# Performance work log

Measured on AMD Instinct MI355X. Metric: run time of the kernel, lower is better.

Reference implementation:

```python
import jax, jax.numpy as jnp
import numpy as np

EPS = 1e-3          # posdef_tol
CRLB = 1.0          # contraction_rate_lb
STD = 0.5           # initialization_std
DX, L, DIN, DOUT, B = 512, 512, 256, 256, 8192


def setup_inputs() -> dict:
    key = jax.random.key(0)
    ks = jax.random.split(key, 9)
    f32 = jnp.float32
    return {
        "u_in": jax.random.normal(ks[0], (B, 1, DIN), f32),
        "x0": jnp.zeros((B, 1, DX), f32),
        "X": jax.random.normal(ks[1], (2 * DX + L, 2 * DX + L), f32) * STD,
        "Y": jax.random.normal(ks[2], (DX, DX), f32) * STD,
        "B2": jax.random.normal(ks[3], (DX, DIN), f32) * STD,
        "C2": jax.random.normal(ks[4], (DOUT, DX), f32) * STD,
        "D21": jax.random.normal(ks[5], (DOUT, L), f32) * STD,
        "D22": jax.random.normal(ks[6], (DOUT, DIN), f32) * STD,
        "D12": jax.random.normal(ks[7], (L, DIN), f32) * STD,
    }


def _derive(X, Y, dx, l):
    # update_model_param: H = X^T X + eps*I, then block-split
    H = X.T @ X + EPS * jnp.eye(2 * dx + l, dtype=X.dtype)
    H11 = H[:dx, :dx]
    H21 = H[dx:dx + l, :dx]
    H22 = H[dx:dx + l, dx:dx + l]
    H31 = H[dx + l:, :dx]
    H32 = H[dx + l:, dx:dx + l]
    H33 = H[dx + l:, dx + l:]
    Fm = H31
    B1 = H32
    E = 0.5 * (H11 + CRLB * H33 + Y - Y.T)
    Lam = 0.5 * jnp.diag(H22)
    D11 = -jnp.tril(H22, -1)   # strictly lower triangular
    C1 = -H21
    return Fm, B1, E, Lam, D11, C1


def reference(u_in, x0, X, Y, B2, C2, D21, D22, D12):
    b = u_in.shape[0]
    dx = x0.shape[-1]
    l = D12.shape[0]
    u = u_in[:, 0, :]          # (B, din)
    x = x0[:, 0, :]            # (B, dx)
    Fm, B1, E, Lam, D11, C1 = _derive(X, Y, dx, l)

    # v_i = C1[i]@x + D11[i]@w + D12[i]@u ; the x/u parts are loop-invariant
    a = x @ C1.T + u @ D12.T   # (B, l)

    def step(w, inputs):
        a_i, d_row, lam_i, e_row = inputs
        v = a_i + w @ d_row                       # (B,) forward substitution
        w = w + jnp.tanh(v / lam_i)[:, None] * e_row[None, :]
        return w, None

    eye = jnp.eye(l, dtype=u.dtype)
    w0 = jnp.zeros((b, l), u.dtype)
    w, _ = jax.lax.scan(step, w0, (a.T, D11, Lam, eye))  # (B, l)

    pre = x @ Fm.T + w @ B1.T + u @ B2.T          # (B, dx)
    # F.linear(pre, E^{-1}) = pre @ E^{-T} = solve(E, pre^T)^T
    x_new = jnp.linalg.solve(E, pre.T).T          # (B, dx)
    y = x_new @ C2.T + w @ D21.T + u @ D22.T      # (B, dout)
    return y[:, None, :]                          # (B, 1, dout)
```

## Files before the change

kernel.cpp:

```cpp
#include <hip/hip_runtime.h>
#include <cstdint>
#include <cstddef>

#define EPSC 0.001f

typedef __attribute__((ext_vector_type(8))) short short8;
typedef __attribute__((ext_vector_type(4))) float f32x4;

__device__ inline void bsplit(float f, ushort& h, ushort& l) {
  uint b = __float_as_uint(f);
  h = (ushort)(b >> 16);
  float r = f - __uint_as_float(b & 0xFFFF0000u);
  l = (ushort)(__float_as_uint(r) >> 16);
}

__global__ void k_anynz(const float* __restrict__ x, int n4, int* __restrict__ flag) {
  int i = blockIdx.x * blockDim.x + threadIdx.x;
  int stride = gridDim.x * blockDim.x;
  int found = 0;
  for (; i < n4; i += stride) {
    float4 v = ((const float4*)x)[i];
    if (v.x != 0.f || v.y != 0.f || v.z != 0.f || v.w != 0.f) { found = 1; break; }
  }
  if (found) atomicOr(flag, 1);
}

__global__ __launch_bounds__(256) void k_tsplit(const float* __restrict__ src,
    ushort* __restrict__ dh, ushort* __restrict__ dl, int R, int C)
{
  __shared__ float t[32][33];
  const int c0 = blockIdx.x * 32, r0 = blockIdx.y * 32;
  const int tid = threadIdx.x;
  const int lr = tid >> 3, lc4 = (tid & 7) * 4;
  float4 v = *(const float4*)(src + (size_t)(r0 + lr) * C + c0 + lc4);
  t[lr][lc4 + 0] = v.x; t[lr][lc4 + 1] = v.y;
  t[lr][lc4 + 2] = v.z; t[lr][lc4 + 3] = v.w;
  __syncthreads();
  ushort4 hv, lv;
  float f;
  f = t[lc4 + 0][lr]; bsplit(f, hv.x, lv.x);
  f = t[lc4 + 1][lr]; bsplit(f, hv.y, lv.y);
  f = t[lc4 + 2][lr]; bsplit(f, hv.z, lv.z);
  f = t[lc4 + 3][lr]; bsplit(f, hv.w, lv.w);
  size_t off = (size_t)(c0 + lr) * R + r0 + lc4;
  *(ushort4*)(dh + off) = hv;
  *(ushort4*)(dl + off) = lv;
}

__global__ void k_split2(const float* __restrict__ s0, ushort* __restrict__ h0,
                         ushort* __restrict__ l0, int c0,
                         const float* __restrict__ s1, ushort* __restrict__ h1,
                         ushort* __restrict__ l1, int c1)
{
  int i = blockIdx.x * 256 + threadIdx.x;
  int tot = c0 + c1;
  int stride = gridDim.x * 256;
  for (; i < tot; i += stride) {
    const float* s; ushort* h; ushort* l; int k;
    if (i < c0) { s = s0; h = h0; l = l0; k = i; }
    else        { s = s1; h = h1; l = l1; k = i - c0; }
    float4 v = ((const float4*)s)[k];
    ushort4 hv, lv;
    bsplit(v.x, hv.x, lv.x);
    bsplit(v.y, hv.y, lv.y);
    bsplit(v.z, hv.z, lv.z);
    bsplit(v.w, hv.w, lv.w);
    ((ushort4*)h)[k] = hv;
    ((ushort4*)l)[k] = lv;
  }
}

__global__ __launch_bounds__(256) void k_xtxm(
    const ushort* __restrict__ Xth, const ushort* __restrict__ Xtl,
    const float* __restrict__ Y,
    float* __restrict__ E, float* __restrict__ C1,
    float* __restrict__ D11, float* __restrict__ D11T, float* __restrict__ Lam,
    ushort* __restrict__ FmTh, ushort* __restrict__ FmTl,
    ushort* __restrict__ B1Th, ushort* __restrict__ B1Tl)
{
  __shared__ ushort sAh[64][40], sAl[64][40], sBh[64][40], sBl[64][40];
  const int z = blockIdx.z;
  int aOff[2], bOff[2], nops;
  switch (z) {
    case 0:  aOff[0] = 0;    bOff[0] = 0;    aOff[1] = 1024; bOff[1] = 1024; nops = 2; break;
    case 1:  aOff[0] = 512;  bOff[0] = 0;    nops = 1; break;
    case 2:  aOff[0] = 512;  bOff[0] = 512;  nops = 1; break;
    case 3:  aOff[0] = 0;    bOff[0] = 1024; nops = 1; break;
    default: aOff[0] = 512;  bOff[0] = 1024; nops = 1; break;
  }
  const int tid = threadIdx.x;
  const int m0 = blockIdx.x * 64, n0 = blockIdx.y * 64;
  const int wid = tid >> 6, lane = tid & 63;
  const int wr = wid >> 1, wc = wid & 1;
  const int fr = lane & 15, fg = lane >> 4;
  const int srow = tid >> 2;
  const int sko = (tid & 3) * 8;
  f32x4 acc[2][2] = {};
  const int K = 1536;

  for (int op = 0; op < nops; ++op) {
    const ushort* Ah = Xth + (size_t)(aOff[op]) * K;
    const ushort* Al = Xtl + (size_t)(aOff[op]) * K;
    const ushort* Bh = Xth + (size_t)(bOff[op]) * K;
    const ushort* Bl = Xtl + (size_t)(bOff[op]) * K;
    uint4 pah = *(const uint4*)(Ah + (size_t)(m0 + srow) * K + sko);
    uint4 pal = *(const uint4*)(Al + (size_t)(m0 + srow) * K + sko);
    uint4 pbh = *(const uint4*)(Bh + (size_t)(n0 + srow) * K + sko);
    uint4 pbl = *(const uint4*)(Bl + (size_t)(n0 + srow) * K + sko);
    for (int k0 = 0; k0 < K; k0 += 32) {
      __syncthreads();
      *(uint4*)&sAh[srow][sko] = pah;
      *(uint4*)&sAl[srow][sko] = pal;
      *(uint4*)&sBh[srow][sko] = pbh;
      *(uint4*)&sBl[srow][sko] = pbl;
      __syncthreads();
      if (k0 + 32 < K) {
        pah = *(const uint4*)(Ah + (size_t)(m0 + srow) * K + k0 + 32 + sko);
        pal = *(const uint4*)(Al + (size_t)(m0 + srow) * K + k0 + 32 + sko);
        pbh = *(const uint4*)(Bh + (size_t)(n0 + srow) * K + k0 + 32 + sko);
        pbl = *(const uint4*)(Bl + (size_t)(n0 + srow) * K + k0 + 32 + sko);
      }
      short8 fah[2], fal[2], fbh[2], fbl[2];
#pragma unroll
      for (int s = 0; s < 2; ++s) {
        fah[s] = *(const short8*)&sAh[wr * 32 + s * 16 + fr][fg * 8];
        fal[s] = *(const short8*)&sAl[wr * 32 + s * 16 + fr][fg * 8];
        fbh[s] = *(const short8*)&sBh[wc * 32 + s * 16 + fr][fg * 8];
        fbl[s] = *(const short8*)&sBl[wc * 32 + s * 16 + fr][fg * 8];
      }
#pragma unroll
      for (int i = 0; i < 2; ++i)
#pragma unroll
        for (int j = 0; j < 2; ++j) {
          acc[i][j] = __builtin_amdgcn_mfma_f32_16x16x32_bf16(fah[i], fbh[j], acc[i][j], 0, 0, 0);
          acc[i][j] = __builtin_amdgcn_mfma_f32_16x16x32_bf16(fah[i], fbl[j], acc[i][j], 0, 0, 0);
          acc[i][j] = __builtin_amdgcn_mfma_f32_16x16x32_bf16(fal[i], fbh[j], acc[i][j], 0, 0, 0);
        }
    }
  }

#pragma unroll
  for (int i = 0; i < 2; ++i)
#pragma unroll
    for (int j = 0; j < 2; ++j) {
      int rbase = m0 + wr * 32 + i * 16 + fg * 4;
      int cc = n0 + wc * 32 + j * 16 + fr;
#pragma unroll
      for (int q = 0; q < 4; ++q) {
        int rr = rbase + q;
        float d = acc[i][j][q];
        size_t idx = (size_t)rr * 512 + cc;
        if (z == 0) {
          float o = 0.5f * (d + Y[idx] - Y[(size_t)cc * 512 + rr]);
          if (rr == cc) o += EPSC;
          E[idx] = o;
        } else if (z == 1) {
          C1[idx] = -d;
        } else if (z == 2) {
          float o = (cc < rr) ? -d : 0.f;
          D11[idx] = o;
          D11T[(size_t)cc * 512 + rr] = o;
          if (rr == cc) Lam[rr] = 0.5f * (d + EPSC);
        } else if (z == 3) {
          ushort h, l; bsplit(d, h, l);
          FmTh[idx] = h; FmTl[idx] = l;
        } else {
          ushort h, l; bsplit(d, h, l);
          B1Th[idx] = h; B1Tl[idx] = l;
        }
      }
    }
}

__global__ void k_nsinit(const float* __restrict__ E, const float* __restrict__ C2,
    float* __restrict__ Tf, ushort* __restrict__ Th, ushort* __restrict__ Tl,
    ushort* __restrict__ Tth, ushort* __restrict__ Ttl,
    float* __restrict__ Qf, ushort* __restrict__ Qh, ushort* __restrict__ Ql)
{
  int g = blockIdx.x * 256 + threadIdx.x;
  int row = g >> 7;
  int c4 = (g & 127) << 2;
  float s0 = 0.85f / E[(size_t)(c4 + 0) * 513];
  float s1 = 0.85f / E[(size_t)(c4 + 1) * 513];
  float s2 = 0.85f / E[(size_t)(c4 + 2) * 513];
  float s3 = 0.85f / E[(size_t)(c4 + 3) * 513];
  if (row < 512) {
    float4 v = *(const float4*)(E + (size_t)row * 512 + c4);
    v.x *= s0; v.y *= s1; v.z *= s2; v.w *= s3;
    *(float4*)(Tf + (size_t)row * 512 + c4) = v;
    ushort4 hv, lv;
    bsplit(v.x, hv.x, lv.x); bsplit(v.y, hv.y, lv.y);
    bsplit(v.z, hv.z, lv.z); bsplit(v.w, hv.w, lv.w);
    *(ushort4*)(Th + (size_t)row * 512 + c4) = hv;
    *(ushort4*)(Tl + (size_t)row * 512 + c4) = lv;
    Tth[(size_t)(c4 + 0) * 512 + row] = hv.x; Ttl[(size_t)(c4 + 0) * 512 + row] = lv.x;
    Tth[(size_t)(c4 + 1) * 512 + row] = hv.y; Ttl[(size_t)(c4 + 1) * 512 + row] = lv.y;
    Tth[(size_t)(c4 + 2) * 512 + row] = hv.z; Ttl[(size_t)(c4 + 2) * 512 + row] = lv.z;
    Tth[(size_t)(c4 + 3) * 512 + row] = hv.w; Ttl[(size_t)(c4 + 3) * 512 + row] = lv.w;
  } else {
    int qr = row - 512;
    float4 v = *(const float4*)(C2 + (size_t)qr * 512 + c4);
    v.x *= s0; v.y *= s1; v.z *= s2; v.w *= s3;
    *(float4*)(Qf + (size_t)qr * 512 + c4) = v;
    ushort4 hv, lv;
    bsplit(v.x, hv.x, lv.x); bsplit(v.y, hv.y, lv.y);
    bsplit(v.z, hv.z, lv.z); bsplit(v.w, hv.w, lv.w);
    *(ushort4*)(Qh + (size_t)qr * 512 + c4) = hv;
    *(ushort4*)(Ql + (size_t)qr * 512 + c4) = lv;
  }
}

template <bool WITH_T>
__global__ __launch_bounds__(256) void k_nsm(
    const ushort* __restrict__ Th, const ushort* __restrict__ Tl,
    const ushort* __restrict__ Tth, const ushort* __restrict__ Ttl,
    const ushort* __restrict__ Qh, const ushort* __restrict__ Ql,
    const float* __restrict__ Tprev, const float* __restrict__ Qprev,
    float* __restrict__ Tnext, ushort* __restrict__ Thn, ushort* __restrict__ Tln,
    ushort* __restrict__ Tthn, ushort* __restrict__ Ttln,
    float* __restrict__ Qnext, ushort* __restrict__ Qhn, ushort* __restrict__ Qln)
{
  __shared__ ushort sAh[64][40], sAl[64][40], sBh[64][40], sBl[64][40];
  const int tid = threadIdx.x;
  const int yy = blockIdx.y;
  const bool isT = WITH_T && (yy < 8);
  const int m0 = (isT ? yy : (yy - (WITH_T ? 8 : 0))) * 64;
  const int n0 = blockIdx.x * 64;
  const ushort* Ah = isT ? Th : Qh;
  const ushort* Al = isT ? Tl : Ql;
  const int wid = tid >> 6, lane = tid & 63;
  const int wr = wid >> 1, wc = wid & 1;
  const int fr = lane & 15, fg = lane >> 4;
  const int srow = tid >> 2;
  const int sko = (tid & 3) * 8;
  const int K = 512;
  f32x4 acc[2][2] = {};

  uint4 pah = *(const uint4*)(Ah + (size_t)(m0 + srow) * K + sko);
  uint4 pal = *(const uint4*)(Al + (size_t)(m0 + srow) * K + sko);
  uint4 pbh = *(const uint4*)(Tth + (size_t)(n0 + srow) * K + sko);
  uint4 pbl = *(const uint4*)(Ttl + (size_t)(n0 + srow) * K + sko);
  for (int k0 = 0; k0 < K; k0 += 32) {
    __syncthreads();
    *(uint4*)&sAh[srow][sko] = pah;
    *(uint4*)&sAl[srow][sko] = pal;
    *(uint4*)&sBh[srow][sko] = pbh;
    *(uint4*)&sBl[srow][sko] = pbl;
    __syncthreads();
    if (k0 + 32 < K) {
      pah = *(const uint4*)(Ah + (size_t)(m0 + srow) * K + k0 + 32 + sko);
      pal = *(const uint4*)(Al + (size_t)(m0 + srow) * K + k0 + 32 + sko);
      pbh = *(const uint4*)(Tth + (size_t)(n0 + srow) * K + k0 + 32 + sko);
      pbl = *(const uint4*)(Ttl + (size_t)(n0 + srow) * K + k0 + 32 + sko);
    }
    short8 fah[2], fal[2], fbh[2], fbl[2];
#pragma unroll
    for (int s = 0; s < 2; ++s) {
      fah[s] = *(const short8*)&sAh[wr * 32 + s * 16 + fr][fg * 8];
      fal[s] = *(const short8*)&sAl[wr * 32 + s * 16 + fr][fg * 8];
      fbh[s] = *(const short8*)&sBh[wc * 32 + s * 16 + fr][fg * 8];
      fbl[s] = *(const short8*)&sBl[wc * 32 + s * 16 + fr][fg * 8];
    }
#pragma unroll
    for (int i = 0; i < 2; ++i)
#pragma unroll
      for (int j = 0; j < 2; ++j) {
        acc[i][j] = __builtin_amdgcn_mfma_f32_16x16x32_bf16(fah[i], fbh[j], acc[i][j], 0, 0, 0);
        acc[i][j] = __builtin_amdgcn_mfma_f32_16x16x32_bf16(fah[i], fbl[j], acc[i][j], 0, 0, 0);
        acc[i][j] = __builtin_amdgcn_mfma_f32_16x16x32_bf16(fal[i], fbh[j], acc[i][j], 0, 0, 0);
      }
  }

#pragma unroll
  for (int i = 0; i < 2; ++i)
#pragma unroll
    for (int j = 0; j < 2; ++j) {
      int rbase = m0 + wr * 32 + i * 16 + fg * 4;
      int cc = n0 + wc * 32 + j * 16 + fr;
#pragma unroll
      for (int q = 0; q < 4; ++q) {
        int rr = rbase + q;
        size_t idx = (size_t)rr * 512 + cc;
        ushort h, l;
        if (isT) {
          float tn = 2.f * Tprev[idx] - acc[i][j][q];
          Tnext[idx] = tn;
          bsplit(tn, h, l);
          Thn[idx] = h; Tln[idx] = l;
          Tthn[(size_t)cc * 512 + rr] = h; Ttln[(size_t)cc * 512 + rr] = l;
        } else {
          float qn = 2.f * Qprev[idx] - acc[i][j][q];
          Qnext[idx] = qn;
          bsplit(qn, h, l);
          Qhn[idx] = h; Qln[idx] = l;
        }
      }
    }
}

__global__ __launch_bounds__(256) void k_foldm(
    const ushort* __restrict__ Qh, const ushort* __restrict__ Ql,
    const ushort* __restrict__ FmTh, const ushort* __restrict__ FmTl,
    const ushort* __restrict__ B1Th, const ushort* __restrict__ B1Tl,
    const ushort* __restrict__ B2Th, const ushort* __restrict__ B2Tl,
    const float* __restrict__ D21, const float* __restrict__ D22,
    float* __restrict__ P1, ushort* __restrict__ P2h, ushort* __restrict__ P2l,
    ushort* __restrict__ P3h, ushort* __restrict__ P3l)
{
  __shared__ ushort sAh[64][40], sAl[64][40], sBh[64][40], sBl[64][40];
  const int z = blockIdx.z;
  const int N = (z == 2) ? 256 : 512;
  const int n0 = blockIdx.x * 64;
  if (n0 >= N) return;
  const ushort* Bh = (z == 0) ? FmTh : (z == 1) ? B1Th : B2Th;
  const ushort* Bl = (z == 0) ? FmTl : (z == 1) ? B1Tl : B2Tl;
  const int tid = threadIdx.x;
  const int m0 = blockIdx.y * 64;
  const int wid = tid >> 6, lane = tid & 63;
  const int wr = wid >> 1, wc = wid & 1;
  const int fr = lane & 15, fg = lane >> 4;
  const int srow = tid >> 2;
  const int sko = (tid & 3) * 8;
  const int K = 512;
  f32x4 acc[2][2] = {};

  uint4 pah = *(const uint4*)(Qh + (size_t)(m0 + srow) * K + sko);
  uint4 pal = *(const uint4*)(Ql + (size_t)(m0 + srow) * K + sko);
  uint4 pbh = *(const uint4*)(Bh + (size_t)(n0 + srow) * K + sko);
  uint4 pbl = *(const uint4*)(Bl + (size_t)(n0 + srow) * K + sko);
  for (int k0 = 0; k0 < K; k0 += 32) {
    __syncthreads();
    *(uint4*)&sAh[srow][sko] = pah;
    *(uint4*)&sAl[srow][sko] = pal;
    *(uint4*)&sBh[srow][sko] = pbh;
    *(uint4*)&sBl[srow][sko] = pbl;
    __syncthreads();
    if (k0 + 32 < K) {
      pah = *(const uint4*)(Qh + (size_t)(m0 + srow) * K + k0 + 32 + sko);
      pal = *(const uint4*)(Ql + (size_t)(m0 + srow) * K + k0 + 32 + sko);
      pbh = *(const uint4*)(Bh + (size_t)(n0 + srow) * K + k0 + 32 + sko);
      pbl = *(const uint4*)(Bl + (size_t)(n0 + srow) * K + k0 + 32 + sko);
    }
    short8 fah[2], fal[2], fbh[2], fbl[2];
#pragma unroll
    for (int s = 0; s < 2; ++s) {
      fah[s] = *(const short8*)&sAh[wr * 32 + s * 16 + fr][fg * 8];
      fal[s] = *(const short8*)&sAl[wr * 32 + s * 16 + fr][fg * 8];
      fbh[s] = *(const short8*)&sBh[wc * 32 + s * 16 + fr][fg * 8];
      fbl[s] = *(const short8*)&sBl[wc * 32 + s * 16 + fr][fg * 8];
    }
#pragma unroll
    for (int i = 0; i < 2; ++i)
#pragma unroll
      for (int j = 0; j < 2; ++j) {
        acc[i][j] = __builtin_amdgcn_mfma_f32_16x16x32_bf16(fah[i], fbh[j], acc[i][j], 0, 0, 0);
        acc[i][j] = __builtin_amdgcn_mfma_f32_16x16x32_bf16(fah[i], fbl[j], acc[i][j], 0, 0, 0);
        acc[i][j] = __builtin_amdgcn_mfma_f32_16x16x32_bf16(fal[i], fbh[j], acc[i][j], 0, 0, 0);
      }
  }

#pragma unroll
  for (int i = 0; i < 2; ++i)
#pragma unroll
    for (int j = 0; j < 2; ++j) {
      int rbase = m0 + wr * 32 + i * 16 + fg * 4;
      int cc = n0 + wc * 32 + j * 16 + fr;
#pragma unroll
      for (int q = 0; q < 4; ++q) {
        int rr = rbase + q;
        float d = acc[i][j][q];
        if (z == 0) {
          P1[(size_t)rr * 512 + cc] = d;
        } else if (z == 1) {
          size_t idx = (size_t)rr * 512 + cc;
          float p = d + D21[idx];
          ushort h, l; bsplit(p, h, l);
          P2h[idx] = h; P2l[idx] = l;
        } else {
          size_t idx = (size_t)rr * 256 + cc;
          float p = d + D22[idx];
          ushort h, l; bsplit(p, h, l);
          P3h[idx] = h; P3l[idx] = l;
        }
      }
    }
}

template <int NOPS>
__global__ __launch_bounds__(256) void k_ntm(
    const ushort* __restrict__ Ah0, const ushort* __restrict__ Al0,
    const ushort* __restrict__ Bh0, const ushort* __restrict__ Bl0, int K0,
    const ushort* __restrict__ Ah1, const ushort* __restrict__ Al1,
    const ushort* __restrict__ Bh1, const ushort* __restrict__ Bl1, int K1,
    float* __restrict__ C, int ldc)
{
  __shared__ ushort sAh[64][40], sAl[64][40], sBh[64][40], sBl[64][40];
  const int tid = threadIdx.x;
  const int m0 = blockIdx.x * 64, n0 = blockIdx.y * 64;
  const int wid = tid >> 6, lane = tid & 63;
  const int wr = wid >> 1, wc = wid & 1;
  const int fr = lane & 15, fg = lane >> 4;
  const int srow = tid >> 2;
  const int sko = (tid & 3) * 8;
  f32x4 acc[2][2] = {};

#pragma unroll
  for (int op = 0; op < NOPS; ++op) {
    const ushort* Ah = (op == 0) ? Ah0 : Ah1;
    const ushort* Al = (op == 0) ? Al0 : Al1;
    const ushort* Bh = (op == 0) ? Bh0 : Bh1;
    const ushort* Bl = (op == 0) ? Bl0 : Bl1;
    const int K = (op == 0) ? K0 : K1;
    uint4 pah = *(const uint4*)(Ah + (size_t)(m0 + srow) * K + sko);
    uint4 pal = *(const uint4*)(Al + (size_t)(m0 + srow) * K + sko);
    uint4 pbh = *(const uint4*)(Bh + (size_t)(n0 + srow) * K + sko);
    uint4 pbl = *(const uint4*)(Bl + (size_t)(n0 + srow) * K + sko);
    for (int k0 = 0; k0 < K; k0 += 32) {
      __syncthreads();
      *(uint4*)&sAh[srow][sko] = pah;
      *(uint4*)&sAl[srow][sko] = pal;
      *(uint4*)&sBh[srow][sko] = pbh;
      *(uint4*)&sBl[srow][sko] = pbl;
      __syncthreads();
      if (k0 + 32 < K) {
        pah = *(const uint4*)(Ah + (size_t)(m0 + srow) * K + k0 + 32 + sko);
        pal = *(const uint4*)(Al + (size_t)(m0 + srow) * K + k0 + 32 + sko);
        pbh = *(const uint4*)(Bh + (size_t)(n0 + srow) * K + k0 + 32 + sko);
        pbl = *(const uint4*)(Bl + (size_t)(n0 + srow) * K + k0 + 32 + sko);
      }
      short8 fah[2], fal[2], fbh[2], fbl[2];
#pragma unroll
      for (int s = 0; s < 2; ++s) {
        fah[s] = *(const short8*)&sAh[wr * 32 + s * 16 + fr][fg * 8];
        fal[s] = *(const short8*)&sAl[wr * 32 + s * 16 + fr][fg * 8];
        fbh[s] = *(const short8*)&sBh[wc * 32 + s * 16 + fr][fg * 8];
        fbl[s] = *(const short8*)&sBl[wc * 32 + s * 16 + fr][fg * 8];
      }
#pragma unroll
      for (int i = 0; i < 2; ++i)
#pragma unroll
        for (int j = 0; j < 2; ++j) {
          acc[i][j] = __builtin_amdgcn_mfma_f32_16x16x32_bf16(fah[i], fbh[j], acc[i][j], 0, 0, 0);
          acc[i][j] = __builtin_amdgcn_mfma_f32_16x16x32_bf16(fah[i], fbl[j], acc[i][j], 0, 0, 0);
          acc[i][j] = __builtin_amdgcn_mfma_f32_16x16x32_bf16(fal[i], fbh[j], acc[i][j], 0, 0, 0);
        }
    }
  }

#pragma unroll
  for (int i = 0; i < 2; ++i)
#pragma unroll
    for (int j = 0; j < 2; ++j) {
      int rr = m0 + wr * 32 + i * 16 + fg * 4;
      int cc = n0 + wc * 32 + j * 16 + fr;
#pragma unroll
      for (int q = 0; q < 4; ++q)
        C[(size_t)(rr + q) * ldc + cc] = acc[i][j][q];
    }
}

__global__ __launch_bounds__(256) void k_ntadd(const float* __restrict__ A,
    const float* __restrict__ B, int K, const int* __restrict__ flag,
    float* __restrict__ C, int ldc)
{
  if (*flag == 0) return;
  __shared__ float As[16][68];
  __shared__ float Bs[16][68];
  const int tid = threadIdx.x;
  const int tx = tid & 15, ty = tid >> 4;
  const int m0 = blockIdx.x * 64, n0 = blockIdx.y * 64;
  const int lr = tid >> 2;
  const int lk = (tid & 3) * 4;
  float acc[4][4];
#pragma unroll
  for (int i = 0; i < 4; ++i)
#pragma unroll
    for (int j = 0; j < 4; ++j) acc[i][j] = 0.f;
  float4 av = *(const float4*)(A + (size_t)(m0 + lr) * K + lk);
  float4 bv = *(const float4*)(B + (size_t)(n0 + lr) * K + lk);
  for (int k0 = 0; k0 < K; k0 += 16) {
    __syncthreads();
    As[lk + 0][lr] = av.x; As[lk + 1][lr] = av.y;
    As[lk + 2][lr] = av.z; As[lk + 3][lr] = av.w;
    Bs[lk + 0][lr] = bv.x; Bs[lk + 1][lr] = bv.y;
    Bs[lk + 2][lr] = bv.z; Bs[lk + 3][lr] = bv.w;
    __syncthreads();
    if (k0 + 16 < K) {
      av = *(const float4*)(A + (size_t)(m0 + lr) * K + k0 + 16 + lk);
      bv = *(const float4*)(B + (size_t)(n0 + lr) * K + k0 + 16 + lk);
    }
#pragma unroll
    for (int kk = 0; kk < 16; ++kk) {
      float4 a4 = *(const float4*)&As[kk][4 * ty];
      float4 b4 = *(const float4*)&Bs[kk][4 * tx];
      float ar[4] = {a4.x, a4.y, a4.z, a4.w};
      float br[4] = {b4.x, b4.y, b4.z, b4.w};
#pragma unroll
      for (int i = 0; i < 4; ++i)
#pragma unroll
        for (int j = 0; j < 4; ++j)
          acc[i][j] = fmaf(ar[i], br[j], acc[i][j]);
    }
  }
#pragma unroll
  for (int i = 0; i < 4; ++i) {
    float* p = C + (size_t)(m0 + 4 * ty + i) * ldc + n0 + 4 * tx;
    float4 v = *(float4*)p;
    v.x += acc[i][0]; v.y += acc[i][1]; v.z += acc[i][2]; v.w += acc[i][3];
    *(float4*)p = v;
  }
}

__global__ __launch_bounds__(512, 4) void k_scan(const float* __restrict__ a,
    const float* __restrict__ D11, const float* __restrict__ D11T,
    const float* __restrict__ Lam, ushort* __restrict__ wh, ushort* __restrict__ wl)
{
  __shared__ float wt[512][17];
  __shared__ float sblk[32][17];
  __shared__ float shist[6][32][17];
  __shared__ float dblkT[2][32][33];
  __shared__ float doff[32][33];
  __shared__ float ablk[32][17];
  __shared__ float rl2[512];
  const int tid = threadIdx.x;
  const int row0 = blockIdx.x * 16;

  rl2[tid] = 2.f / Lam[tid];
  if (tid < 128) {
    int rr = tid >> 3, cq = (tid & 7) * 4;
    float4 v = *(const float4*)(a + (size_t)(row0 + rr) * 512 + cq);
    sblk[cq + 0][rr] = v.x; sblk[cq + 1][rr] = v.y;
    sblk[cq + 2][rr] = v.z; sblk[cq + 3][rr] = v.w;
  } else if (tid < 384) {
    int f = tid - 128;
    int rr = f >> 3, cq = (f & 7) * 4;
    float4 v = *(const float4*)(D11 + (size_t)rr * 512 + cq);
    dblkT[0][cq + 0][rr] = v.x; dblkT[0][cq + 1][rr] = v.y;
    dblkT[0][cq + 2][rr] = v.z; dblkT[0][cq + 3][rr] = v.w;
  }
  __syncthreads();

  for (int t = 0; t < 16; ++t) {
    const int wv = tid >> 6;
    const int lane = tid & 63;
    const int c0 = 32 * t;
    const int jend2 = 32 * (t + 1);
    if (wv == 0) {
      if (lane < 16) {
        float s[32];
#pragma unroll
        for (int il = 0; il < 32; ++il) s[il] = sblk[il][lane];
#pragma unroll
        for (int il = 0; il < 32; ++il) {
          float x2 = s[il] * rl2[c0 + il];
          float e = __expf(x2);
          float wv2 = 1.f - 2.f * __builtin_amdgcn_rcpf(e + 1.f);
          wt[c0 + il][lane] = wv2;
#pragma unroll
          for (int j2 = il + 1; j2 < 32; ++j2)
            s[j2] = fmaf(dblkT[t & 1][il][j2], wv2, s[j2]);
        }
      }
    } else if (wv <= 6) {
      if (t < 15) {
        const int r = lane & 15;
        const int il0 = (lane >> 4) * 8;
        const int n = c0;
        float acc[8] = {0.f, 0.f, 0.f, 0.f, 0.f, 0.f, 0.f, 0.f};
        for (int j0 = (wv - 1) * 4; j0 < n; j0 += 24) {
          float4 d[4][2];
          float wj4[4];
#pragma unroll
          for (int q = 0; q < 4; ++q) {
            int j = j0 + q;
            int jc = (j < n) ? j : 0;
            const float* dp = D11T + (size_t)jc * 512 + jend2 + il0;
            d[q][0] = *(const float4*)dp;
            d[q][1] = *(const float4*)(dp + 4);
            wj4[q] = (j < n) ? wt[j][r] : 0.f;
          }
#pragma unroll
          for (int q = 0; q < 4; ++q) {
            acc[0] = fmaf(d[q][0].x, wj4[q], acc[0]);
            acc[1] = fmaf(d[q][0].y, wj4[q], acc[1]);
            acc[2] = fmaf(d[q][0].z, wj4[q], acc[2]);
            acc[3] = fmaf(d[q][0].w, wj4[q], acc[3]);
            acc[4] = fmaf(d[q][1].x, wj4[q], acc[4]);
            acc[5] = fmaf(d[q][1].y, wj4[q], acc[5]);
            acc[6] = fmaf(d[q][1].z, wj4[q], acc[6]);
            acc[7] = fmaf(d[q][1].w, wj4[q], acc[7]);
          }
        }
#pragma unroll
        for (int k = 0; k < 8; ++k) shist[wv - 1][il0 + k][r] = acc[k];
      }
    } else {
      if (t < 15) {
#pragma unroll
        for (int e = 0; e < 4; ++e) {
          int f = lane + 64 * e;
          int rr = f >> 3, cq = (f & 7) * 4;
          float4 v = *(const float4*)(D11 + (size_t)(jend2 + rr) * 512 + c0 + cq);
          doff[rr][cq + 0] = v.x; doff[rr][cq + 1] = v.y;
          doff[rr][cq + 2] = v.z; doff[rr][cq + 3] = v.w;
          float4 v2 = *(const float4*)(D11 + (size_t)(jend2 + rr) * 512 + jend2 + cq);
          dblkT[(t + 1) & 1][cq + 0][rr] = v2.x; dblkT[(t + 1) & 1][cq + 1][rr] = v2.y;
          dblkT[(t + 1) & 1][cq + 2][rr] = v2.z; dblkT[(t + 1) & 1][cq + 3][rr] = v2.w;
        }
#pragma unroll
        for (int e = 0; e < 2; ++e) {
          int f = lane + 64 * e;
          int rr = f >> 3, cq = (f & 7) * 4;
          float4 v = *(const float4*)(a + (size_t)(row0 + rr) * 512 + jend2 + cq);
          ablk[cq + 0][rr] = v.x; ablk[cq + 1][rr] = v.y;
          ablk[cq + 2][rr] = v.z; ablk[cq + 3][rr] = v.w;
        }
      }
    }
    __syncthreads();
    if (t < 15) {
      const int il = tid >> 4, r2 = tid & 15;
      float s = ablk[il][r2];
#pragma unroll
      for (int k = 0; k < 6; ++k) s += shist[k][il][r2];
#pragma unroll 8
      for (int j = 0; j < 32; ++j)
        s = fmaf(doff[il][j], wt[c0 + j][r2], s);
      sblk[il][r2] = s;
      __syncthreads();
    }
  }

  const int c2 = tid & 255;
  const int rh = tid >> 8;
#pragma unroll
  for (int k = 0; k < 8; ++k) {
    int row = rh * 8 + k;
    float f0 = wt[2 * c2][row];
    float f1 = wt[2 * c2 + 1][row];
    ushort h0, l0, h1, l1;
    bsplit(f0, h0, l0);
    bsplit(f1, h1, l1);
    size_t off = (size_t)(row0 + row) * 512 + 2 * c2;
    *(ushort2*)(wh + off) = make_ushort2(h0, h1);
    *(ushort2*)(wl + off) = make_ushort2(l0, l1);
  }
}

extern "C" void kernel_launch(void* const* d_in, const int* in_sizes, int n_in,
                              void* d_out, int out_size, void* d_ws, size_t ws_size,
                              hipStream_t stream)
{
  const float* u   = (const float*)d_in[0];
  const float* x0  = (const float*)d_in[1];
  const float* X   = (const float*)d_in[2];
  const float* Y   = (const float*)d_in[3];
  const float* B2  = (const float*)d_in[4];
  const float* C2  = (const float*)d_in[5];
  const float* D21 = (const float*)d_in[6];
  const float* D22 = (const float*)d_in[7];
  const float* D12 = (const float*)d_in[8];
  float* out = (float*)d_out;
  float* ws = (float*)d_ws;

  float*  E    = ws + 0;
  float*  C1   = ws + 262144;
  float*  D11  = ws + 524288;
  float*  D11T = ws + 786432;
  float*  Lam  = ws + 1048576;
  int*    flag = (int*)(ws + 1049088);
  float*  Tf0  = ws + 1049600;
  float*  Tf1  = ws + 1311744;
  float*  Qf0  = ws + 1573888;
  float*  Qf1  = ws + 1704960;
  ushort* Th0  = (ushort*)(ws + 1836032);
  ushort* Tl0  = (ushort*)(ws + 1967104);
  ushort* Tth0 = (ushort*)(ws + 2098176);
  ushort* Ttl0 = (ushort*)(ws + 2229248);
  ushort* Th1  = (ushort*)(ws + 2360320);
  ushort* Tl1  = (ushort*)(ws + 2491392);
  ushort* Tth1 = (ushort*)(ws + 2622464);
  ushort* Ttl1 = (ushort*)(ws + 2753536);
  ushort* Qh0  = (ushort*)(ws + 2884608);
  ushort* Ql0  = (ushort*)(ws + 2950144);
  ushort* Qh1  = (ushort*)(ws + 3015680);
  ushort* Ql1  = (ushort*)(ws + 3081216);
  ushort* FmTh = (ushort*)(ws + 3146752);
  ushort* FmTl = (ushort*)(ws + 3277824);
  ushort* B1Th = (ushort*)(ws + 3408896);
  ushort* B1Tl = (ushort*)(ws + 3539968);
  ushort* B2Th = (ushort*)(ws + 3671040);
  ushort* B2Tl = (ushort*)(ws + 3736576);
  float*  P1   = ws + 3802112;
  ushort* P2h  = (ushort*)(ws + 3933184);
  ushort* P2l  = (ushort*)(ws + 3998720);
  ushort* P3h  = (ushort*)(ws + 4064256);
  ushort* P3l  = (ushort*)(ws + 4097024);
  ushort* D12h = (ushort*)(ws + 4129792);
  ushort* D12l = (ushort*)(ws + 4195328);
  ushort* uh   = (ushort*)(ws + 4260864);
  ushort* ul   = (ushort*)(ws + 5309440);
  float*  abuf = ws + 6358016;
  ushort* wh   = (ushort*)(ws + 10552320);
  ushort* wl   = (ushort*)(ws + 12649472);
  ushort* Xth  = (ushort*)(ws + 10552320);
  ushort* Xtl  = (ushort*)(ws + 11731968);

  hipMemsetAsync(flag, 0, 4, stream);
  k_anynz<<<256, 256, 0, stream>>>(x0, 8192 * 512 / 4, flag);

  k_tsplit<<<dim3(48, 48), 256, 0, stream>>>(X, Xth, Xtl, 1536, 1536);
  k_tsplit<<<dim3(8, 16), 256, 0, stream>>>(B2, B2Th, B2Tl, 512, 256);
  k_split2<<<2048, 256, 0, stream>>>(u, uh, ul, 524288, D12, D12h, D12l, 32768);

  k_xtxm<<<dim3(8, 8, 5), 256, 0, stream>>>(Xth, Xtl, Y, E, C1, D11, D11T, Lam,
                                            FmTh, FmTl, B1Th, B1Tl);

  k_ntm<1><<<dim3(128, 8), 256, 0, stream>>>(uh, ul, D12h, D12l, 256,
                                             nullptr, nullptr, nullptr, nullptr, 0,
                                             abuf, 512);
  k_ntadd<<<dim3(128, 8), 256, 0, stream>>>(x0, C1, 512, flag, abuf, 512);

  k_nsinit<<<384, 256, 0, stream>>>(E, C2, Tf0, Th0, Tl0, Tth0, Ttl0, Qf0, Qh0, Ql0);
  ushort *Tha[2] = {Th0, Th1}, *Tla[2] = {Tl0, Tl1};
  ushort *Ttha[2] = {Tth0, Tth1}, *Ttla[2] = {Ttl0, Ttl1};
  ushort *Qha[2] = {Qh0, Qh1}, *Qla[2] = {Ql0, Ql1};
  float *Tfa[2] = {Tf0, Tf1}, *Qfa[2] = {Qf0, Qf1};
  int cur = 0;
  for (int it = 0; it < 5; ++it) {
    int nxt = cur ^ 1;
    k_nsm<true><<<dim3(8, 12), 256, 0, stream>>>(
        Tha[cur], Tla[cur], Ttha[cur], Ttla[cur], Qha[cur], Qla[cur],
        Tfa[cur], Qfa[cur],
        Tfa[nxt], Tha[nxt], Tla[nxt], Ttha[nxt], Ttla[nxt],
        Qfa[nxt], Qha[nxt], Qla[nxt]);
    cur = nxt;
  }
  int nxt = cur ^ 1;
  k_nsm<false><<<dim3(8, 4), 256, 0, stream>>>(
      Tha[cur], Tla[cur], Ttha[cur], Ttla[cur], Qha[cur], Qla[cur],
      Tfa[cur], Qfa[cur],
      Tfa[nxt], Tha[nxt], Tla[nxt], Ttha[nxt], Ttla[nxt],
      Qfa[nxt], Qha[nxt], Qla[nxt]);
  ushort* Qh = Qha[nxt];
  ushort* Ql = Qla[nxt];

  k_foldm<<<dim3(8, 4, 3), 256, 0, stream>>>(Qh, Ql, FmTh, FmTl, B1Th, B1Tl,
                                             B2Th, B2Tl, D21, D22,
                                             P1, P2h, P2l, P3h, P3l);

  k_scan<<<512, 512, 0, stream>>>(abuf, D11, D11T, Lam, wh, wl);

  k_ntm<2><<<dim3(128, 4), 256, 0, stream>>>(wh, wl, P2h, P2l, 512,
                                             uh, ul, P3h, P3l, 256,
                                             out, 256);
  k_ntadd<<<dim3(128, 4), 256, 0, stream>>>(x0, P1, 512, flag, out, 256);
}
```

Measured before the change: 438.7 us.

## Use split-bf16 MFMA for scan history update and store w as bf16 pairs

The history-accumulation warps in the sequential scan kernel now compute the off-block D11·w contribution with bf16 MFMA instructions using a hi/lo split (three products), instead of scalar FMAs over a transposed fp32 D11. To support this, the D11 producer now emits hi/lo bf16 copies instead of a transposed fp32 copy. The scan keeps w in shared memory as bf16 hi/lo arrays plus a small fp32 current-block buffer, so the final write-out becomes a plain copy. This is meant to cut the FMA and global-load cost of the history phase, but drops the lo·lo term and changes the LDS layout.

Result: faster. 406.8 us (-7.3%).

```diff
diff --git a/kernel.cpp b/kernel.cpp
--- a/kernel.cpp
+++ b/kernel.cpp
@@ -74,7 +74,8 @@
     const ushort* __restrict__ Xth, const ushort* __restrict__ Xtl,
     const float* __restrict__ Y,
     float* __restrict__ E, float* __restrict__ C1,
-    float* __restrict__ D11, float* __restrict__ D11T, float* __restrict__ Lam,
+    float* __restrict__ D11, ushort* __restrict__ D11h, ushort* __restrict__ D11l,
+    float* __restrict__ Lam,
     ushort* __restrict__ FmTh, ushort* __restrict__ FmTl,
     ushort* __restrict__ B1Th, ushort* __restrict__ B1Tl)
 {
@@ -159,7 +160,8 @@
         } else if (z == 2) {
           float o = (cc < rr) ? -d : 0.f;
           D11[idx] = o;
-          D11T[(size_t)cc * 512 + rr] = o;
+          ushort h, l; bsplit(o, h, l);
+          D11h[idx] = h; D11l[idx] = l;
           if (rr == cc) Lam[rr] = 0.5f * (d + EPSC);
         } else if (z == 3) {
           ushort h, l; bsplit(d, h, l);
@@ -512,10 +514,13 @@
 }
 
 __global__ __launch_bounds__(512, 4) void k_scan(const float* __restrict__ a,
-    const float* __restrict__ D11, const float* __restrict__ D11T,
+    const float* __restrict__ D11,
+    const ushort* __restrict__ D11h, const ushort* __restrict__ D11l,
     const float* __restrict__ Lam, ushort* __restrict__ wh, ushort* __restrict__ wl)
 {
-  __shared__ float wt[512][17];
+  __shared__ ushort wth[16][520];
+  __shared__ ushort wtl[16][520];
+  __shared__ float wcur[32][17];
   __shared__ float sblk[32][17];
   __shared__ float shist[6][32][17];
   __shared__ float dblkT[2][32][33];
@@ -540,11 +545,13 @@
   }
   __syncthreads();
 
+  const int wv = tid >> 6;
+  const int lane = tid & 63;
+  const int fr = lane & 15, fg = lane >> 4;
+
   for (int t = 0; t < 16; ++t) {
-    const int wv = tid >> 6;
-    const int lane = tid & 63;
     const int c0 = 32 * t;
-    const int jend2 = 32 * (t + 1);
+    const int jend2 = c0 + 32;
     if (wv == 0) {
       if (lane < 16) {
         float s[32];
@@ -554,45 +561,41 @@
         for (int il = 0; il < 32; ++il) {
           float x2 = s[il] * rl2[c0 + il];
           float e = __expf(x2);
-          float wv2 = 1.f - 2.f * __builtin_amdgcn_rcpf(e + 1.f);
-          wt[c0 + il][lane] = wv2;
+          float w2 = 1.f - 2.f * __builtin_amdgcn_rcpf(e + 1.f);
+          wcur[il][lane] = w2;
+          ushort hh, ll; bsplit(w2, hh, ll);
+          wth[lane][c0 + il] = hh;
+          wtl[lane][c0 + il] = ll;
 #pragma unroll
           for (int j2 = il + 1; j2 < 32; ++j2)
-            s[j2] = fmaf(dblkT[t & 1][il][j2], wv2, s[j2]);
+            s[j2] = fmaf(dblkT[t & 1][il][j2], w2, s[j2]);
         }
       }
     } else if (wv <= 6) {
       if (t < 15) {
-        const int r = lane & 15;
-        const int il0 = (lane >> 4) * 8;
-        const int n = c0;
-        float acc[8] = {0.f, 0.f, 0.f, 0.f, 0.f, 0.f, 0.f, 0.f};
-        for (int j0 = (wv - 1) * 4; j0 < n; j0 += 24) {
-          float4 d[4][2];
-          float wj4[4];
-#pragma unroll
-          for (int q = 0; q < 4; ++q) {
-            int j = j0 + q;
-            int jc = (j < n) ? j : 0;
-            const float* dp = D11T + (size_t)jc * 512 + jend2 + il0;
-            d[q][0] = *(const float4*)dp;
-            d[q][1] = *(const float4*)(dp + 4);
-            wj4[q] = (j < n) ? wt[j][r] : 0.f;
-          }
-#pragma unroll
-          for (int q = 0; q < 4; ++q) {
-            acc[0] = fmaf(d[q][0].x, wj4[q], acc[0]);
-            acc[1] = fmaf(d[q][0].y, wj4[q], acc[1]);
-            acc[2] = fmaf(d[q][0].z, wj4[q], acc[2]);
-            acc[3] = fmaf(d[q][0].w, wj4[q], acc[3]);
-            acc[4] = fmaf(d[q][1].x, wj4[q], acc[4]);
-            acc[5] = fmaf(d[q][1].y, wj4[q], acc[5]);
-            acc[6] = fmaf(d[q][1].z, wj4[q], acc[6]);
-            acc[7] = fmaf(d[q][1].w, wj4[q], acc[7]);
-          }
-        }
-#pragma unroll
-        for (int k = 0; k < 8; ++k) shist[wv - 1][il0 + k][r] = acc[k];
+        f32x4 acc0 = {}, acc1 = {};
+        for (int s = wv - 1; s < t; s += 6) {
+          const int jb = 32 * s;
+          const size_t ao0 = (size_t)(jend2 + fr) * 512 + jb + fg * 8;
+          const size_t ao1 = (size_t)(jend2 + 16 + fr) * 512 + jb + fg * 8;
+          short8 a0h = *(const short8*)(D11h + ao0);
+          short8 a0l = *(const short8*)(D11l + ao0);
+          short8 a1h = *(const short8*)(D11h + ao1);
+          short8 a1l = *(const short8*)(D11l + ao1);
+          short8 bh = *(const short8*)&wth[fr][jb + fg * 8];
+          short8 bl = *(const short8*)&wtl[fr][jb + fg * 8];
+          acc0 = __builtin_amdgcn_mfma_f32_16x16x32_bf16(a0h, bh, acc0, 0, 0, 0);
+          acc0 = __builtin_amdgcn_mfma_f32_16x16x32_bf16(a0h, bl, acc0, 0, 0, 0);
+          acc0 = __builtin_amdgcn_mfma_f32_16x16x32_bf16(a0l, bh, acc0, 0, 0, 0);
+          acc1 = __builtin_amdgcn_mfma_f32_16x16x32_bf16(a1h, bh, acc1, 0, 0, 0);
+          acc1 = __builtin_amdgcn_mfma_f32_16x16x32_bf16(a1h, bl, acc1, 0, 0, 0);
+          acc1 = __builtin_amdgcn_mfma_f32_16x16x32_bf16(a1l, bh, acc1, 0, 0, 0);
+        }
+#pragma unroll
+        for (int q = 0; q < 4; ++q) {
+          shist[wv - 1][fg * 4 + q][fr] = acc0[q];
+          shist[wv - 1][16 + fg * 4 + q][fr] = acc1[q];
+        }
       }
     } else {
       if (t < 15) {
@@ -625,25 +628,20 @@
       for (int k = 0; k < 6; ++k) s += shist[k][il][r2];
 #pragma unroll 8
       for (int j = 0; j < 32; ++j)
-        s = fmaf(doff[il][j], wt[c0 + j][r2], s);
+        s = fmaf(doff[il][j], wcur[j][r2], s);
       sblk[il][r2] = s;
       __syncthreads();
     }
   }
 
-  const int c2 = tid & 255;
-  const int rh = tid >> 8;
-#pragma unroll
-  for (int k = 0; k < 8; ++k) {
-    int row = rh * 8 + k;
-    float f0 = wt[2 * c2][row];
-    float f1 = wt[2 * c2 + 1][row];
-    ushort h0, l0, h1, l1;
-    bsplit(f0, h0, l0);
-    bsplit(f1, h1, l1);
-    size_t off = (size_t)(row0 + row) * 512 + 2 * c2;
-    *(ushort2*)(wh + off) = make_ushort2(h0, h1);
-    *(ushort2*)(wl + off) = make_ushort2(l0, l1);
+  const int k2 = tid & 255;
+  const int rb = tid >> 8;
+#pragma unroll
+  for (int p = 0; p < 8; ++p) {
+    int r = rb * 8 + p;
+    size_t off = (size_t)(row0 + r) * 512 + 2 * k2;
+    *(uint*)(wh + off) = *(const uint*)&wth[r][2 * k2];
+    *(uint*)(wl + off) = *(const uint*)&wtl[r][2 * k2];
   }
 }
 
@@ -666,7 +664,8 @@
   float*  E    = ws + 0;
   float*  C1   = ws + 262144;
   float*  D11  = ws + 524288;
-  float*  D11T = ws + 786432;
+  ushort* D11h = (ushort*)(ws + 786432);
+  ushort* D11l = (ushort*)(ws + 917504);
   float*  Lam  = ws + 1048576;
   int*    flag = (int*)(ws + 1049088);
   float*  Tf0  = ws + 1049600;
@@ -713,7 +712,8 @@
   k_tsplit<<<dim3(8, 16), 256, 0, stream>>>(B2, B2Th, B2Tl, 512, 256);
   k_split2<<<2048, 256, 0, stream>>>(u, uh, ul, 524288, D12, D12h, D12l, 32768);
 
-  k_xtxm<<<dim3(8, 8, 5), 256, 0, stream>>>(Xth, Xtl, Y, E, C1, D11, D11T, Lam,
+  k_xtxm<<<dim3(8, 8, 5), 256, 0, stream>>>(Xth, Xtl, Y, E, C1,
+                                            D11, D11h, D11l, Lam,
                                             FmTh, FmTl, B1Th, B1Tl);
 
   k_ntm<1><<<dim3(128, 8), 256, 0, stream>>>(uh, ul, D12h, D12l, 256,
@@ -749,7 +749,7 @@
                                              B2Th, B2Tl, D21, D22,
                                              P1, P2h, P2l, P3h, P3l);
 
-  k_scan<<<512, 512, 0, stream>>>(abuf, D11, D11T, Lam, wh, wl);
+  k_scan<<<512, 512, 0, stream>>>(abuf, D11, D11h, D11l, Lam, wh, wl);
 
   k_ntm<2><<<dim3(128, 4), 256, 0, stream>>>(wh, wl, P2h, P2l, 512,
                                              uh, ul, P3h, P3l, 256,
```
